# Optimization experiments

Hardware: AMD Instinct MI355X
Metric: run time of the kernel (lower is better)

## Reference

```python
import jax, jax.numpy as jnp
import numpy as np

B, NH, NKV, HD, SW, D = 32, 32, 8, 128, 4096, 4096
G = NH // NKV  # GQA group size


def setup_inputs() -> dict:
    key = jax.random.key(0)
    ks = jax.random.split(key, 7)
    x = jax.random.normal(ks[0], (1, 1, B, D), jnp.float32)
    wqkv = jax.random.normal(ks[1], (D, NH * HD + 2 * NKV * HD), jnp.float32) * 0.02
    wo = jax.random.normal(ks[2], (D, D), jnp.float32) * 0.02
    rot_mat = jax.random.normal(ks[3], (HD, HD), jnp.float32) * 0.1
    cache_k = jax.random.normal(ks[4], (B, NKV, SW, HD), jnp.float32)
    cache_v = jax.random.normal(ks[5], (B, NKV, SW, HD), jnp.float32)
    attn_mask = jnp.zeros((1, NH, B, SW), jnp.float32)
    return {"x": x, "wqkv": wqkv, "wo": wo, "rot_mat": rot_mat,
            "cache_k": cache_k, "cache_v": cache_v,
            "attn_mask": attn_mask, "current_pos": 4095}


def reference(x, wqkv, wo, rot_mat, cache_k, cache_v, attn_mask, current_pos):
    # start_pos advanced to 4096 -> padded_layer_past_len = layer_slice = SW (full window)
    scale = jnp.asarray(HD, x.dtype) ** -0.5
    # fused QKV projection: (B, D) @ (D, 6144)
    xqkv = x[0, 0] @ wqkv  # (B, NH*HD + 2*NKV*HD)
    q = xqkv[:, : NH * HD].reshape(B, NH, HD)
    k = xqkv[:, NH * HD: NH * HD + NKV * HD].reshape(B, NKV, HD)
    v = xqkv[:, NH * HD + NKV * HD:].reshape(B, NKV, HD)
    # matrix-form rotary embedding for the current position
    q = q @ rot_mat  # (B, NH, HD)
    k = k @ rot_mat  # (B, NKV, HD)
    # KV-cache update at current_pos
    keys = cache_k.at[:, :, current_pos, :].set(k)    # (B, NKV, SW, HD)
    values = cache_v.at[:, :, current_pos, :].set(v)  # (B, NKV, SW, HD)
    # GQA sliding-window attention over the (full) window
    qg = (q * scale).reshape(B, NKV, G, HD)
    scores = jnp.einsum('bkgd,bksd->bkgs', qg, keys)  # (B, NKV, G, SW)
    mask = jnp.transpose(attn_mask[0], (1, 0, 2)).reshape(B, NKV, G, SW)
    probs = jax.nn.softmax(scores + mask, axis=-1)
    ctx = jnp.einsum('bkgs,bksd->bkgd', probs, values)  # (B, NKV, G, HD)
    # concatenate heads + output projection
    out = ctx.reshape(B, NH * HD) @ wo  # (B, D)
    return out.reshape(1, 1, B, D)
```

## Files before the change

kernel.cpp:

```cpp
#include <hip/hip_runtime.h>

#define BB 32
#define NHH 32
#define NKVV 8
#define HDD 128
#define SWW 4096
#define DD 4096
#define GG 4
#define QKVC 6144
#define NSPLIT 16
#define CHUNK (SWW / NSPLIT)
#define KSPB 16

__global__ __launch_bounds__(256) void skinny_gemm_part(
    const float* __restrict__ x, const float* __restrict__ w,
    float* __restrict__ part, int K, int ncols) {
  __shared__ float2 red[4][64][8];
  const int t = threadIdx.x;
  const int ct = t & 63, kg = t >> 6;
  const long c0 = (long)blockIdx.x * 128 + ct * 2;
  const int Kb = K / KSPB;
  const int klen = Kb / 4;
  const int k0 = blockIdx.y * Kb + kg * klen;
  float2 acc[BB];
#pragma unroll
  for (int r = 0; r < BB; ++r) acc[r] = make_float2(0.f, 0.f);

  for (int k = k0; k < k0 + klen; k += 4) {
    float2 wv0 = *(const float2*)&w[(long)(k + 0) * ncols + c0];
    float2 wv1 = *(const float2*)&w[(long)(k + 1) * ncols + c0];
    float2 wv2 = *(const float2*)&w[(long)(k + 2) * ncols + c0];
    float2 wv3 = *(const float2*)&w[(long)(k + 3) * ncols + c0];
#pragma unroll
    for (int r = 0; r < BB; ++r) {
      float4 xv = *(const float4*)&x[r * K + k];
      acc[r].x = fmaf(xv.x, wv0.x, acc[r].x);
      acc[r].y = fmaf(xv.x, wv0.y, acc[r].y);
      acc[r].x = fmaf(xv.y, wv1.x, acc[r].x);
      acc[r].y = fmaf(xv.y, wv1.y, acc[r].y);
      acc[r].x = fmaf(xv.z, wv2.x, acc[r].x);
      acc[r].y = fmaf(xv.z, wv2.y, acc[r].y);
      acc[r].x = fmaf(xv.w, wv3.x, acc[r].x);
      acc[r].y = fmaf(xv.w, wv3.y, acc[r].y);
    }
  }
  for (int rc = 0; rc < 4; ++rc) {
    if (rc) __syncthreads();
#pragma unroll
    for (int j = 0; j < 8; ++j) red[kg][ct][j] = acc[rc * 8 + j];
    __syncthreads();
    if (kg == 0) {
#pragma unroll
      for (int j = 0; j < 8; ++j) {
        float2 s0 = red[0][ct][j], s1 = red[1][ct][j];
        float2 s2 = red[2][ct][j], s3 = red[3][ct][j];
        float2 sm = make_float2((s0.x + s1.x) + (s2.x + s3.x),
                                (s0.y + s1.y) + (s2.y + s3.y));
        *(float2*)&part[((long)blockIdx.y * BB + rc * 8 + j) * ncols + c0] = sm;
      }
    }
  }
}

__global__ __launch_bounds__(256) void reduce_part(
    const float* __restrict__ part, float* __restrict__ out, long n) {
  long i = (long)blockIdx.x * 256 + threadIdx.x;
  if (i >= n) return;
  float s = 0.f;
#pragma unroll
  for (int j = 0; j < KSPB; ++j) s += part[(long)j * n + i];
  out[i] = s;
}

__global__ __launch_bounds__(128) void rotary_kernel(
    const float* __restrict__ xqkv, const float* __restrict__ rot,
    float* __restrict__ q_rot, float* __restrict__ k_rot) {
  __shared__ float vec[HDD];
  const int blk = blockIdx.x;
  const int j = threadIdx.x;
  const float* src;
  float* dst;
  if (blk < BB * NHH) {
    int b = blk >> 5, h = blk & 31;
    src = xqkv + (long)b * QKVC + h * HDD;
    dst = q_rot + (long)(b * NHH + h) * HDD;
  } else {
    int i = blk - BB * NHH;
    int b = i >> 3, kv = i & 7;
    src = xqkv + (long)b * QKVC + NHH * HDD + kv * HDD;
    dst = k_rot + (long)(b * NKVV + kv) * HDD;
  }
  vec[j] = src[j];
  __syncthreads();
  float a0 = 0.f, a1 = 0.f, a2 = 0.f, a3 = 0.f;
#pragma unroll
  for (int d0 = 0; d0 < HDD; d0 += 4) {
    a0 += vec[d0 + 0] * rot[(d0 + 0) * HDD + j];
    a1 += vec[d0 + 1] * rot[(d0 + 1) * HDD + j];
    a2 += vec[d0 + 2] * rot[(d0 + 2) * HDD + j];
    a3 += vec[d0 + 3] * rot[(d0 + 3) * HDD + j];
  }
  dst[j] = (a0 + a1) + (a2 + a3);
}

__global__ __launch_bounds__(256) void attn_partial(
    const float* __restrict__ q_rot, const float* __restrict__ k_rot,
    const float* __restrict__ xqkv, const float* __restrict__ cache_k,
    const float* __restrict__ cache_v, const float* __restrict__ mask,
    const int* __restrict__ curpos, float* __restrict__ pm,
    float* __restrict__ pl, float* __restrict__ pacc) {
  __shared__ float4 scp[CHUNK];
  __shared__ float4 mkp[CHUNK];
  __shared__ float red[4][GG][HDD];

  const int blk = blockIdx.x;
  const int split = blk & (NSPLIT - 1);
  const int bkv = blk >> 4;
  const int b = bkv >> 3, kv = bkv & 7;
  const int cur = curpos[0];
  const int s0 = split * CHUNK;
  const int t = threadIdx.x, lane = t & 63, w = t >> 6;
  const int lg = lane & 15;
  const float scale = 0.08838834764831845f;

  for (int i = t; i < GG * CHUNK; i += 256) {
    int g = i >> 8;
    int sl = i & (CHUNK - 1);
    ((float*)mkp)[sl * 4 + g] =
        mask[((long)(kv * GG + g) * BB + b) * SWW + s0 + sl];
  }

  float4 qa[GG], qb[GG];
#pragma unroll
  for (int g = 0; g < GG; ++g) {
    const float4* qp =
        (const float4*)(q_rot + (long)((b * NHH + kv * GG + g) * HDD));
    qa[g] = qp[lg];
    qb[g] = qp[lg + 16];
  }
  const float* kbase = cache_k + (long)(b * NKVV + kv) * SWW * HDD;
  const float* knew = k_rot + (long)(b * NKVV + kv) * HDD;
  __syncthreads();

#pragma unroll 2
  for (int it = 0; it < CHUNK / 16; ++it) {
    int sloc = it * 16 + w * 4 + (lane >> 4);
    int s = s0 + sloc;
    const float4* kp =
        (const float4*)((s == cur) ? knew : (kbase + (long)s * HDD));
    float4 ka = kp[lg];
    float4 kb = kp[lg + 16];
    float dots[GG];
#pragma unroll
    for (int g = 0; g < GG; ++g) {
      dots[g] = ka.x * qa[g].x + ka.y * qa[g].y + ka.z * qa[g].z +
                ka.w * qa[g].w + kb.x * qb[g].x + kb.y * qb[g].y +
                kb.z * qb[g].z + kb.w * qb[g].w;
    }
#pragma unroll
    for (int m = 1; m < 16; m <<= 1) {
#pragma unroll
      for (int g = 0; g < GG; ++g) dots[g] += __shfl_xor(dots[g], m);
    }
    if (lg == 0) {
      float4 mv = mkp[sloc];
      float4 sv;
      sv.x = fmaf(dots[0], scale, mv.x);
      sv.y = fmaf(dots[1], scale, mv.y);
      sv.z = fmaf(dots[2], scale, mv.z);
      sv.w = fmaf(dots[3], scale, mv.w);
      scp[sloc] = sv;
    }
  }
  __syncthreads();

  const int sl = w * 64 + lane;
  float4 e = scp[sl];
  float4 mx = e;
#pragma unroll
  for (int m = 1; m < 64; m <<= 1) {
    mx.x = fmaxf(mx.x, __shfl_xor(mx.x, m));
    mx.y = fmaxf(mx.y, __shfl_xor(mx.y, m));
    mx.z = fmaxf(mx.z, __shfl_xor(mx.z, m));
    mx.w = fmaxf(mx.w, __shfl_xor(mx.w, m));
  }
  if (lane == 0) *(float4*)&red[w][0][0] = mx;
  __syncthreads();
  float4 m0 = *(const float4*)&red[0][0][0];
  float4 m1 = *(const float4*)&red[1][0][0];
  float4 m2 = *(const float4*)&red[2][0][0];
  float4 m3 = *(const float4*)&red[3][0][0];
  float4 Mx;
  Mx.x = fmaxf(fmaxf(m0.x, m1.x), fmaxf(m2.x, m3.x));
  Mx.y = fmaxf(fmaxf(m0.y, m1.y), fmaxf(m2.y, m3.y));
  Mx.z = fmaxf(fmaxf(m0.z, m1.z), fmaxf(m2.z, m3.z));
  Mx.w = fmaxf(fmaxf(m0.w, m1.w), fmaxf(m2.w, m3.w));
  float4 p;
  p.x = __expf(e.x - Mx.x);
  p.y = __expf(e.y - Mx.y);
  p.z = __expf(e.z - Mx.z);
  p.w = __expf(e.w - Mx.w);
  scp[sl] = p;
  float4 sm = p;
#pragma unroll
  for (int m = 1; m < 64; m <<= 1) {
    sm.x += __shfl_xor(sm.x, m);
    sm.y += __shfl_xor(sm.y, m);
    sm.z += __shfl_xor(sm.z, m);
    sm.w += __shfl_xor(sm.w, m);
  }
  if (lane == 0) *(float4*)&red[w][1][0] = sm;
  __syncthreads();
  float4 t0 = *(const float4*)&red[0][1][0];
  float4 t1 = *(const float4*)&red[1][1][0];
  float4 t2 = *(const float4*)&red[2][1][0];
  float4 t3 = *(const float4*)&red[3][1][0];
  if (t == 0) {
    long base = ((long)(b * NHH + kv * GG)) * NSPLIT + split;
    pm[base + 0 * NSPLIT] = Mx.x;
    pm[base + 1 * NSPLIT] = Mx.y;
    pm[base + 2 * NSPLIT] = Mx.z;
    pm[base + 3 * NSPLIT] = Mx.w;
    pl[base + 0 * NSPLIT] = (t0.x + t1.x) + (t2.x + t3.x);
    pl[base + 1 * NSPLIT] = (t0.y + t1.y) + (t2.y + t3.y);
    pl[base + 2 * NSPLIT] = (t0.z + t1.z) + (t2.z + t3.z);
    pl[base + 3 * NSPLIT] = (t0.w + t1.w) + (t2.w + t3.w);
  }
  __syncthreads();

  const float* vbase = cache_v + (long)(b * NKVV + kv) * SWW * HDD;
  const float* vnew =
      xqkv + (long)b * QKVC + NHH * HDD + NKVV * HDD + kv * HDD;
  const int dl = lane & 31;
  const int half = lane >> 5;
  float4 acc0 = make_float4(0, 0, 0, 0), acc1 = acc0, acc2 = acc0,
         acc3 = acc0;
#pragma unroll 4
  for (int it = 0; it < 32; ++it) {
    int slp = w * 64 + it * 2 + half;
    float4 v4 = *(const float4*)(vbase + (long)(s0 + slp) * HDD + dl * 4);
    float4 p4 = scp[slp];
    acc0.x = fmaf(p4.x, v4.x, acc0.x);
    acc0.y = fmaf(p4.x, v4.y, acc0.y);
    acc0.z = fmaf(p4.x, v4.z, acc0.z);
    acc0.w = fmaf(p4.x, v4.w, acc0.w);
    acc1.x = fmaf(p4.y, v4.x, acc1.x);
    acc1.y = fmaf(p4.y, v4.y, acc1.y);
    acc1.z = fmaf(p4.y, v4.z, acc1.z);
    acc1.w = fmaf(p4.y, v4.w, acc1.w);
    acc2.x = fmaf(p4.z, v4.x, acc2.x);
    acc2.y = fmaf(p4.z, v4.y, acc2.y);
    acc2.z = fmaf(p4.z, v4.z, acc2.z);
    acc2.w = fmaf(p4.z, v4.w, acc2.w);
    acc3.x = fmaf(p4.w, v4.x, acc3.x);
    acc3.y = fmaf(p4.w, v4.y, acc3.y);
    acc3.z = fmaf(p4.w, v4.z, acc3.z);
    acc3.w = fmaf(p4.w, v4.w, acc3.w);
  }
  if (cur >= s0 && cur < s0 + CHUNK) {
    int slc = cur - s0;
    if (w == (slc >> 6) && half == (slc & 1)) {
      float4 p4 = scp[slc];
      float4 vc = *(const float4*)(vbase + (long)cur * HDD + dl * 4);
      float4 vn = *(const float4*)(vnew + dl * 4);
      float4 d;
      d.x = vn.x - vc.x;
      d.y = vn.y - vc.y;
      d.z = vn.z - vc.z;
      d.w = vn.w - vc.w;
      acc0.x = fmaf(p4.x, d.x, acc0.x);
      acc0.y = fmaf(p4.x, d.y, acc0.y);
      acc0.z = fmaf(p4.x, d.z, acc0.z);
      acc0.w = fmaf(p4.x, d.w, acc0.w);
      acc1.x = fmaf(p4.y, d.x, acc1.x);
      acc1.y = fmaf(p4.y, d.y, acc1.y);
      acc1.z = fmaf(p4.y, d.z, acc1.z);
      acc1.w = fmaf(p4.y, d.w, acc1.w);
      acc2.x = fmaf(p4.z, d.x, acc2.x);
      acc2.y = fmaf(p4.z, d.y, acc2.y);
      acc2.z = fmaf(p4.z, d.z, acc2.z);
      acc2.w = fmaf(p4.z, d.w, acc2.w);
      acc3.x = fmaf(p4.w, d.x, acc3.x);
      acc3.y = fmaf(p4.w, d.y, acc3.y);
      acc3.z = fmaf(p4.w, d.z, acc3.z);
      acc3.w = fmaf(p4.w, d.w, acc3.w);
    }
  }
  acc0.x += __shfl_xor(acc0.x, 32);
  acc0.y += __shfl_xor(acc0.y, 32);
  acc0.z += __shfl_xor(acc0.z, 32);
  acc0.w += __shfl_xor(acc0.w, 32);
  acc1.x += __shfl_xor(acc1.x, 32);
  acc1.y += __shfl_xor(acc1.y, 32);
  acc1.z += __shfl_xor(acc1.z, 32);
  acc1.w += __shfl_xor(acc1.w, 32);
  acc2.x += __shfl_xor(acc2.x, 32);
  acc2.y += __shfl_xor(acc2.y, 32);
  acc2.z += __shfl_xor(acc2.z, 32);
  acc2.w += __shfl_xor(acc2.w, 32);
  acc3.x += __shfl_xor(acc3.x, 32);
  acc3.y += __shfl_xor(acc3.y, 32);
  acc3.z += __shfl_xor(acc3.z, 32);
  acc3.w += __shfl_xor(acc3.w, 32);
  if (half == 0) {
    *(float4*)&red[w][0][dl * 4] = acc0;
    *(float4*)&red[w][1][dl * 4] = acc1;
    *(float4*)&red[w][2][dl * 4] = acc2;
    *(float4*)&red[w][3][dl * 4] = acc3;
  }
  __syncthreads();
  if (t < HDD) {
#pragma unroll
    for (int g = 0; g < GG; ++g) {
      float s = (red[0][g][t] + red[1][g][t]) + (red[2][g][t] + red[3][g][t]);
      pacc[(((long)(b * NHH + kv * GG + g)) * NSPLIT + split) * HDD + t] = s;
    }
  }
}

__global__ __launch_bounds__(128) void attn_combine(
    const float* __restrict__ pm, const float* __restrict__ pl,
    const float* __restrict__ pacc, float* __restrict__ ctx) {
  const int bh = blockIdx.x;
  const int d = threadIdx.x;
  float M = -1e30f;
#pragma unroll
  for (int i = 0; i < NSPLIT; ++i) M = fmaxf(M, pm[bh * NSPLIT + i]);
  float L = 0.f, a = 0.f;
#pragma unroll
  for (int i = 0; i < NSPLIT; ++i) {
    float wexp = __expf(pm[bh * NSPLIT + i] - M);
    L += pl[bh * NSPLIT + i] * wexp;
    a += wexp * pacc[((long)bh * NSPLIT + i) * HDD + d];
  }
  ctx[(long)bh * HDD + d] = a / L;
}

extern "C" void kernel_launch(void* const* d_in, const int* in_sizes, int n_in,
                              void* d_out, int out_size, void* d_ws,
                              size_t ws_size, hipStream_t stream) {
  const float* x = (const float*)d_in[0];
  const float* wqkv = (const float*)d_in[1];
  const float* wo = (const float*)d_in[2];
  const float* rot = (const float*)d_in[3];
  const float* cache_k = (const float*)d_in[4];
  const float* cache_v = (const float*)d_in[5];
  const float* mask = (const float*)d_in[6];
  const int* curpos = (const int*)d_in[7];
  float* out = (float*)d_out;

  float* ws = (float*)d_ws;
  float* xqkv = ws;
  float* q_rot = xqkv + 196608;
  float* k_rot = q_rot + 131072;
  float* pm = k_rot + 32768;
  float* pl = pm + 16384;
  float* ctx = pl + 16384;
  float* big = ctx + 131072;
  (void)in_sizes; (void)n_in; (void)out_size; (void)ws_size;

  hipLaunchKernelGGL(skinny_gemm_part, dim3(QKVC / 128, KSPB), dim3(256), 0,
                     stream, x, wqkv, big, DD, QKVC);
  hipLaunchKernelGGL(reduce_part, dim3((BB * QKVC) / 256), dim3(256), 0,
                     stream, big, xqkv, (long)BB * QKVC);
  hipLaunchKernelGGL(rotary_kernel, dim3(BB * NHH + BB * NKVV), dim3(128), 0,
                     stream, xqkv, rot, q_rot, k_rot);
  hipLaunchKernelGGL(attn_partial, dim3(BB * NKVV * NSPLIT), dim3(256), 0,
                     stream, q_rot, k_rot, xqkv, cache_k, cache_v, mask,
                     curpos, pm, pl, big);
  hipLaunchKernelGGL(attn_combine, dim3(BB * NHH), dim3(128), 0, stream, pm,
                     pl, big, ctx);
  hipLaunchKernelGGL(skinny_gemm_part, dim3(DD / 128, KSPB), dim3(256), 0,
                     stream, ctx, wo, big, DD, DD);
  hipLaunchKernelGGL(reduce_part, dim3((BB * DD) / 256), dim3(256), 0, stream,
                     big, out, (long)BB * DD);
}
```

Before: 341.6 us.

## Fuse QK scores, online softmax and PV accumulation in one pass per warp

The attention partial kernel is restructured so each warp streams K and V rows together and keeps a running max/sum with lazy rescaling (threshold 8), instead of writing all scores to shared memory and doing separate max, exp-sum and PV passes with several block barriers. Per-warp partials are merged through shared memory at the end. This aims to overlap K and V loads and remove intermediate syncs, though V is now read as float2 per lane, there are more shuffles per step, and more exps are computed redundantly across lanes. The QKV GEMM loop also gets an unroll-2 pragma.

```diff
diff --git a/kernel.cpp b/kernel.cpp
--- a/kernel.cpp
+++ b/kernel.cpp
@@ -26,6 +26,7 @@
 #pragma unroll
   for (int r = 0; r < BB; ++r) acc[r] = make_float2(0.f, 0.f);
 
+#pragma unroll 2
   for (int k = k0; k < k0 + klen; k += 4) {
     float2 wv0 = *(const float2*)&w[(long)(k + 0) * ncols + c0];
     float2 wv1 = *(const float2*)&w[(long)(k + 1) * ncols + c0];
@@ -103,15 +104,15 @@
   dst[j] = (a0 + a1) + (a2 + a3);
 }
 
-__global__ __launch_bounds__(256) void attn_partial(
+__global__ __launch_bounds__(256) void attn_fused(
     const float* __restrict__ q_rot, const float* __restrict__ k_rot,
     const float* __restrict__ xqkv, const float* __restrict__ cache_k,
     const float* __restrict__ cache_v, const float* __restrict__ mask,
     const int* __restrict__ curpos, float* __restrict__ pm,
     float* __restrict__ pl, float* __restrict__ pacc) {
-  __shared__ float4 scp[CHUNK];
   __shared__ float4 mkp[CHUNK];
-  __shared__ float red[4][GG][HDD];
+  __shared__ float wacc[4][GG][HDD];
+  __shared__ float wml[4][GG][2];
 
   const int blk = blockIdx.x;
   const int split = blk & (NSPLIT - 1);
@@ -121,6 +122,7 @@
   const int s0 = split * CHUNK;
   const int t = threadIdx.x, lane = t & 63, w = t >> 6;
   const int lg = lane & 15;
+  const int grp = lane >> 4;
   const float scale = 0.08838834764831845f;
 
   for (int i = t; i < GG * CHUNK; i += 256) {
@@ -140,16 +142,32 @@
   }
   const float* kbase = cache_k + (long)(b * NKVV + kv) * SWW * HDD;
   const float* knew = k_rot + (long)(b * NKVV + kv) * HDD;
+  const float* vbase = cache_v + (long)(b * NKVV + kv) * SWW * HDD;
+  const float* vnew = xqkv + (long)b * QKVC + NHH * HDD + NKVV * HDD + kv * HDD;
   __syncthreads();
 
-#pragma unroll 2
-  for (int it = 0; it < CHUNK / 16; ++it) {
-    int sloc = it * 16 + w * 4 + (lane >> 4);
-    int s = s0 + sloc;
+  float m0 = -1e30f, m1 = -1e30f, m2 = -1e30f, m3 = -1e30f;
+  float l0 = 0.f, l1 = 0.f, l2 = 0.f, l3 = 0.f;
+  float2 ac0 = make_float2(0, 0), ac1 = ac0, ac2 = ac0, ac3 = ac0;
+  const int d = lane * 2;
+
+  for (int it = 0; it < 16; ++it) {
+    const int sloc = w * 64 + it * 4 + grp;
+    const int s = s0 + sloc;
     const float4* kp =
         (const float4*)((s == cur) ? knew : (kbase + (long)s * HDD));
     float4 ka = kp[lg];
     float4 kb = kp[lg + 16];
+    const int sb = s0 + w * 64 + it * 4;
+    const float* vr0 = (sb + 0 == cur) ? vnew : (vbase + (long)(sb + 0) * HDD);
+    const float* vr1 = (sb + 1 == cur) ? vnew : (vbase + (long)(sb + 1) * HDD);
+    const float* vr2 = (sb + 2 == cur) ? vnew : (vbase + (long)(sb + 2) * HDD);
+    const float* vr3 = (sb + 3 == cur) ? vnew : (vbase + (long)(sb + 3) * HDD);
+    float2 v0 = *(const float2*)(vr0 + d);
+    float2 v1 = *(const float2*)(vr1 + d);
+    float2 v2 = *(const float2*)(vr2 + d);
+    float2 v3 = *(const float2*)(vr3 + d);
+
     float dots[GG];
 #pragma unroll
     for (int g = 0; g < GG; ++g) {
@@ -158,162 +176,94 @@
                 kb.z * qb[g].z + kb.w * qb[g].w;
     }
 #pragma unroll
-    for (int m = 1; m < 16; m <<= 1) {
-#pragma unroll
-      for (int g = 0; g < GG; ++g) dots[g] += __shfl_xor(dots[g], m);
-    }
-    if (lg == 0) {
-      float4 mv = mkp[sloc];
-      float4 sv;
-      sv.x = fmaf(dots[0], scale, mv.x);
-      sv.y = fmaf(dots[1], scale, mv.y);
-      sv.z = fmaf(dots[2], scale, mv.z);
-      sv.w = fmaf(dots[3], scale, mv.w);
-      scp[sloc] = sv;
-    }
+    for (int mm = 1; mm < 16; mm <<= 1) {
+#pragma unroll
+      for (int g = 0; g < GG; ++g) dots[g] += __shfl_xor(dots[g], mm);
+    }
+    float4 mv = mkp[sloc];
+    float4 sv;
+    sv.x = fmaf(dots[0], scale, mv.x);
+    sv.y = fmaf(dots[1], scale, mv.y);
+    sv.z = fmaf(dots[2], scale, mv.z);
+    sv.w = fmaf(dots[3], scale, mv.w);
+    float4 sj0, sj1, sj2, sj3;
+    sj0.x = __shfl(sv.x, 0);  sj0.y = __shfl(sv.y, 0);
+    sj0.z = __shfl(sv.z, 0);  sj0.w = __shfl(sv.w, 0);
+    sj1.x = __shfl(sv.x, 16); sj1.y = __shfl(sv.y, 16);
+    sj1.z = __shfl(sv.z, 16); sj1.w = __shfl(sv.w, 16);
+    sj2.x = __shfl(sv.x, 32); sj2.y = __shfl(sv.y, 32);
+    sj2.z = __shfl(sv.z, 32); sj2.w = __shfl(sv.w, 32);
+    sj3.x = __shfl(sv.x, 48); sj3.y = __shfl(sv.y, 48);
+    sj3.z = __shfl(sv.z, 48); sj3.w = __shfl(sv.w, 48);
+    float nm0 = fmaxf(fmaxf(sj0.x, sj1.x), fmaxf(sj2.x, sj3.x));
+    float nm1 = fmaxf(fmaxf(sj0.y, sj1.y), fmaxf(sj2.y, sj3.y));
+    float nm2 = fmaxf(fmaxf(sj0.z, sj1.z), fmaxf(sj2.z, sj3.z));
+    float nm3 = fmaxf(fmaxf(sj0.w, sj1.w), fmaxf(sj2.w, sj3.w));
+    if (nm0 > m0 + 8.f || nm1 > m1 + 8.f || nm2 > m2 + 8.f ||
+        nm3 > m3 + 8.f) {
+      float M2, f;
+      M2 = fmaxf(m0, nm0); f = __expf(m0 - M2);
+      l0 *= f; ac0.x *= f; ac0.y *= f; m0 = M2;
+      M2 = fmaxf(m1, nm1); f = __expf(m1 - M2);
+      l1 *= f; ac1.x *= f; ac1.y *= f; m1 = M2;
+      M2 = fmaxf(m2, nm2); f = __expf(m2 - M2);
+      l2 *= f; ac2.x *= f; ac2.y *= f; m2 = M2;
+      M2 = fmaxf(m3, nm3); f = __expf(m3 - M2);
+      l3 *= f; ac3.x *= f; ac3.y *= f; m3 = M2;
+    }
+    float p00 = __expf(sj0.x - m0), p10 = __expf(sj1.x - m0),
+          p20 = __expf(sj2.x - m0), p30 = __expf(sj3.x - m0);
+    float p01 = __expf(sj0.y - m1), p11 = __expf(sj1.y - m1),
+          p21 = __expf(sj2.y - m1), p31 = __expf(sj3.y - m1);
+    float p02 = __expf(sj0.z - m2), p12 = __expf(sj1.z - m2),
+          p22 = __expf(sj2.z - m2), p32 = __expf(sj3.z - m2);
+    float p03 = __expf(sj0.w - m3), p13 = __expf(sj1.w - m3),
+          p23 = __expf(sj2.w - m3), p33 = __expf(sj3.w - m3);
+    l0 += (p00 + p10) + (p20 + p30);
+    l1 += (p01 + p11) + (p21 + p31);
+    l2 += (p02 + p12) + (p22 + p32);
+    l3 += (p03 + p13) + (p23 + p33);
+    ac0.x = fmaf(p00, v0.x, fmaf(p10, v1.x, fmaf(p20, v2.x, fmaf(p30, v3.x, ac0.x))));
+    ac0.y = fmaf(p00, v0.y, fmaf(p10, v1.y, fmaf(p20, v2.y, fmaf(p30, v3.y, ac0.y))));
+    ac1.x = fmaf(p01, v0.x, fmaf(p11, v1.x, fmaf(p21, v2.x, fmaf(p31, v3.x, ac1.x))));
+    ac1.y = fmaf(p01, v0.y, fmaf(p11, v1.y, fmaf(p21, v2.y, fmaf(p31, v3.y, ac1.y))));
+    ac2.x = fmaf(p02, v0.x, fmaf(p12, v1.x, fmaf(p22, v2.x, fmaf(p32, v3.x, ac2.x))));
+    ac2.y = fmaf(p02, v0.y, fmaf(p12, v1.y, fmaf(p22, v2.y, fmaf(p32, v3.y, ac2.y))));
+    ac3.x = fmaf(p03, v0.x, fmaf(p13, v1.x, fmaf(p23, v2.x, fmaf(p33, v3.x, ac3.x))));
+    ac3.y = fmaf(p03, v0.y, fmaf(p13, v1.y, fmaf(p23, v2.y, fmaf(p33, v3.y, ac3.y))));
+  }
+
+  wacc[w][0][d] = ac0.x; wacc[w][0][d + 1] = ac0.y;
+  wacc[w][1][d] = ac1.x; wacc[w][1][d + 1] = ac1.y;
+  wacc[w][2][d] = ac2.x; wacc[w][2][d + 1] = ac2.y;
+  wacc[w][3][d] = ac3.x; wacc[w][3][d + 1] = ac3.y;
+  if (lane == 0) {
+    wml[w][0][0] = m0; wml[w][0][1] = l0;
+    wml[w][1][0] = m1; wml[w][1][1] = l1;
+    wml[w][2][0] = m2; wml[w][2][1] = l2;
+    wml[w][3][0] = m3; wml[w][3][1] = l3;
   }
   __syncthreads();
 
-  const int sl = w * 64 + lane;
-  float4 e = scp[sl];
-  float4 mx = e;
-#pragma unroll
-  for (int m = 1; m < 64; m <<= 1) {
-    mx.x = fmaxf(mx.x, __shfl_xor(mx.x, m));
-    mx.y = fmaxf(mx.y, __shfl_xor(mx.y, m));
-    mx.z = fmaxf(mx.z, __shfl_xor(mx.z, m));
-    mx.w = fmaxf(mx.w, __shfl_xor(mx.w, m));
-  }
-  if (lane == 0) *(float4*)&red[w][0][0] = mx;
-  __syncthreads();
-  float4 m0 = *(const float4*)&red[0][0][0];
-  float4 m1 = *(const float4*)&red[1][0][0];
-  float4 m2 = *(const float4*)&red[2][0][0];
-  float4 m3 = *(const float4*)&red[3][0][0];
-  float4 Mx;
-  Mx.x = fmaxf(fmaxf(m0.x, m1.x), fmaxf(m2.x, m3.x));
-  Mx.y = fmaxf(fmaxf(m0.y, m1.y), fmaxf(m2.y, m3.y));
-  Mx.z = fmaxf(fmaxf(m0.z, m1.z), fmaxf(m2.z, m3.z));
-  Mx.w = fmaxf(fmaxf(m0.w, m1.w), fmaxf(m2.w, m3.w));
-  float4 p;
-  p.x = __expf(e.x - Mx.x);
-  p.y = __expf(e.y - Mx.y);
-  p.z = __expf(e.z - Mx.z);
-  p.w = __expf(e.w - Mx.w);
-  scp[sl] = p;
-  float4 sm = p;
-#pragma unroll
-  for (int m = 1; m < 64; m <<= 1) {
-    sm.x += __shfl_xor(sm.x, m);
-    sm.y += __shfl_xor(sm.y, m);
-    sm.z += __shfl_xor(sm.z, m);
-    sm.w += __shfl_xor(sm.w, m);
-  }
-  if (lane == 0) *(float4*)&red[w][1][0] = sm;
-  __syncthreads();
-  float4 t0 = *(const float4*)&red[0][1][0];
-  float4 t1 = *(const float4*)&red[1][1][0];
-  float4 t2 = *(const float4*)&red[2][1][0];
-  float4 t3 = *(const float4*)&red[3][1][0];
-  if (t == 0) {
-    long base = ((long)(b * NHH + kv * GG)) * NSPLIT + split;
-    pm[base + 0 * NSPLIT] = Mx.x;
-    pm[base + 1 * NSPLIT] = Mx.y;
-    pm[base + 2 * NSPLIT] = Mx.z;
-    pm[base + 3 * NSPLIT] = Mx.w;
-    pl[base + 0 * NSPLIT] = (t0.x + t1.x) + (t2.x + t3.x);
-    pl[base + 1 * NSPLIT] = (t0.y + t1.y) + (t2.y + t3.y);
-    pl[base + 2 * NSPLIT] = (t0.z + t1.z) + (t2.z + t3.z);
-    pl[base + 3 * NSPLIT] = (t0.w + t1.w) + (t2.w + t3.w);
-  }
-  __syncthreads();
-
-  const float* vbase = cache_v + (long)(b * NKVV + kv) * SWW * HDD;
-  const float* vnew =
-      xqkv + (long)b * QKVC + NHH * HDD + NKVV * HDD + kv * HDD;
-  const int dl = lane & 31;
-  const int half = lane >> 5;
-  float4 acc0 = make_float4(0, 0, 0, 0), acc1 = acc0, acc2 = acc0,
-         acc3 = acc0;
-#pragma unroll 4
-  for (int it = 0; it < 32; ++it) {
-    int slp = w * 64 + it * 2 + half;
-    float4 v4 = *(const float4*)(vbase + (long)(s0 + slp) * HDD + dl * 4);
-    float4 p4 = scp[slp];
-    acc0.x = fmaf(p4.x, v4.x, acc0.x);
-    acc0.y = fmaf(p4.x, v4.y, acc0.y);
-    acc0.z = fmaf(p4.x, v4.z, acc0.z);
-    acc0.w = fmaf(p4.x, v4.w, acc0.w);
-    acc1.x = fmaf(p4.y, v4.x, acc1.x);
-    acc1.y = fmaf(p4.y, v4.y, acc1.y);
-    acc1.z = fmaf(p4.y, v4.z, acc1.z);
-    acc1.w = fmaf(p4.y, v4.w, acc1.w);
-    acc2.x = fmaf(p4.z, v4.x, acc2.x);
-    acc2.y = fmaf(p4.z, v4.y, acc2.y);
-    acc2.z = fmaf(p4.z, v4.z, acc2.z);
-    acc2.w = fmaf(p4.z, v4.w, acc2.w);
-    acc3.x = fmaf(p4.w, v4.x, acc3.x);
-    acc3.y = fmaf(p4.w, v4.y, acc3.y);
-    acc3.z = fmaf(p4.w, v4.z, acc3.z);
-    acc3.w = fmaf(p4.w, v4.w, acc3.w);
-  }
-  if (cur >= s0 && cur < s0 + CHUNK) {
-    int slc = cur - s0;
-    if (w == (slc >> 6) && half == (slc & 1)) {
-      float4 p4 = scp[slc];
-      float4 vc = *(const float4*)(vbase + (long)cur * HDD + dl * 4);
-      float4 vn = *(const float4*)(vnew + dl * 4);
-      float4 d;
-      d.x = vn.x - vc.x;
-      d.y = vn.y - vc.y;
-      d.z = vn.z - vc.z;
-      d.w = vn.w - vc.w;
-      acc0.x = fmaf(p4.x, d.x, acc0.x);
-      acc0.y = fmaf(p4.x, d.y, acc0.y);
-      acc0.z = fmaf(p4.x, d.z, acc0.z);
-      acc0.w = fmaf(p4.x, d.w, acc0.w);
-      acc1.x = fmaf(p4.y, d.x, acc1.x);
-      acc1.y = fmaf(p4.y, d.y, acc1.y);
-      acc1.z = fmaf(p4.y, d.z, acc1.z);
-      acc1.w = fmaf(p4.y, d.w, acc1.w);
-      acc2.x = fmaf(p4.z, d.x, acc2.x);
-      acc2.y = fmaf(p4.z, d.y, acc2.y);
-      acc2.z = fmaf(p4.z, d.z, acc2.z);
-      acc2.w = fmaf(p4.z, d.w, acc2.w);
-      acc3.x = fmaf(p4.w, d.x, acc3.x);
-      acc3.y = fmaf(p4.w, d.y, acc3.y);
-      acc3.z = fmaf(p4.w, d.z, acc3.z);
-      acc3.w = fmaf(p4.w, d.w, acc3.w);
-    }
-  }
-  acc0.x += __shfl_xor(acc0.x, 32);
-  acc0.y += __shfl_xor(acc0.y, 32);
-  acc0.z += __shfl_xor(acc0.z, 32);
-  acc0.w += __shfl_xor(acc0.w, 32);
-  acc1.x += __shfl_xor(acc1.x, 32);
-  acc1.y += __shfl_xor(acc1.y, 32);
-  acc1.z += __shfl_xor(acc1.z, 32);
-  acc1.w += __shfl_xor(acc1.w, 32);
-  acc2.x += __shfl_xor(acc2.x, 32);
-  acc2.y += __shfl_xor(acc2.y, 32);
-  acc2.z += __shfl_xor(acc2.z, 32);
-  acc2.w += __shfl_xor(acc2.w, 32);
-  acc3.x += __shfl_xor(acc3.x, 32);
-  acc3.y += __shfl_xor(acc3.y, 32);
-  acc3.z += __shfl_xor(acc3.z, 32);
-  acc3.w += __shfl_xor(acc3.w, 32);
-  if (half == 0) {
-    *(float4*)&red[w][0][dl * 4] = acc0;
-    *(float4*)&red[w][1][dl * 4] = acc1;
-    *(float4*)&red[w][2][dl * 4] = acc2;
-    *(float4*)&red[w][3][dl * 4] = acc3;
-  }
-  __syncthreads();
-  if (t < HDD) {
-#pragma unroll
-    for (int g = 0; g < GG; ++g) {
-      float s = (red[0][g][t] + red[1][g][t]) + (red[2][g][t] + red[3][g][t]);
-      pacc[(((long)(b * NHH + kv * GG + g)) * NSPLIT + split) * HDD + t] = s;
+  {
+    const int g = t >> 6;
+    const int dd = (t & 63) * 2;
+    float Mg = fmaxf(fmaxf(wml[0][g][0], wml[1][g][0]),
+                     fmaxf(wml[2][g][0], wml[3][g][0]));
+    float Lg = 0.f, a0 = 0.f, a1 = 0.f;
+#pragma unroll
+    for (int ww = 0; ww < 4; ++ww) {
+      float f = __expf(wml[ww][g][0] - Mg);
+      Lg = fmaf(wml[ww][g][1], f, Lg);
+      a0 = fmaf(f, wacc[ww][g][dd], a0);
+      a1 = fmaf(f, wacc[ww][g][dd + 1], a1);
+    }
+    const long pidx = ((long)(b * NHH + kv * GG + g)) * NSPLIT + split;
+    pacc[pidx * HDD + dd] = a0;
+    pacc[pidx * HDD + dd + 1] = a1;
+    if ((t & 63) == 0) {
+      pm[pidx] = Mg;
+      pl[pidx] = Lg;
     }
   }
 }
@@ -365,7 +315,7 @@
                      stream, big, xqkv, (long)BB * QKVC);
   hipLaunchKernelGGL(rotary_kernel, dim3(BB * NHH + BB * NKVV), dim3(128), 0,
                      stream, xqkv, rot, q_rot, k_rot);
-  hipLaunchKernelGGL(attn_partial, dim3(BB * NKVV * NSPLIT), dim3(256), 0,
+  hipLaunchKernelGGL(attn_fused, dim3(BB * NKVV * NSPLIT), dim3(256), 0,
                      stream, q_rot, k_rot, xqkv, cache_k, cache_v, mask,
                      curpos, pm, pl, big);
   hipLaunchKernelGGL(attn_combine, dim3(BB * NHH), dim3(128), 0, stream, pm,
```

Result: slower. 383.1 us (+12.1%).
